# Kernel optimization log

Hardware: AMD Instinct MI355X
Metric: run time of the kernel (lower is better)

## Reference

```python
import jax, jax.numpy as jnp
import numpy as np

NUM_HEADS = 16
WINDOW = 256  # window_size: each query i attends to keys [max(0, i-W+1), i]


def setup_inputs() -> dict:
    key = jax.random.key(0)
    k1, k2, k3, k4, k5 = jax.random.split(key, 5)
    B, S, D = 2, 4096, 1024
    scale = 0.02
    return {
        "x": jax.random.normal(k1, (B, S, D), dtype=jnp.float32),
        "wq": jax.random.normal(k2, (D, D), dtype=jnp.float32) * scale,
        "wk": jax.random.normal(k3, (D, D), dtype=jnp.float32) * scale,
        "wv": jax.random.normal(k4, (D, D), dtype=jnp.float32) * scale,
        "wo": jax.random.normal(k5, (D, D), dtype=jnp.float32) * scale,
    }


def _sliding_window_attn(x, wq, wk, wv, wo):
    B, S, D = x.shape
    H, W = NUM_HEADS, WINDOW
    Dh = D // H
    nb = S // W  # number of query blocks (S assumed divisible by W)

    def proj(w):
        # nn.Linear: y = x @ w.T ; -> [B, H, nb, W, Dh]
        y = (x @ w.T).reshape(B, nb, W, H, Dh)
        return y.transpose(0, 3, 1, 2, 4)

    q = proj(wq)
    k = proj(wk)
    v = proj(wv)

    # Each query block j attends to key blocks j-1 and j (banded causal window).
    zpad = jnp.zeros((B, H, 1, W, Dh), dtype=x.dtype)
    kpad = jnp.concatenate([zpad, k], axis=2)  # [B,H,nb+1,W,Dh]
    vpad = jnp.concatenate([zpad, v], axis=2)
    k2 = jnp.concatenate([kpad[:, :, :-1], kpad[:, :, 1:]], axis=3)  # [B,H,nb,2W,Dh]
    v2 = jnp.concatenate([vpad[:, :, :-1], vpad[:, :, 1:]], axis=3)

    scores = jnp.einsum("bhjqd,bhjkd->bhjqk", q, k2) / jnp.sqrt(
        jnp.asarray(Dh, dtype=x.dtype)
    )  # [B,H,nb,W,2W]

    # Mask: query global pos i = j*W + qi; key global pos kp = (j-1)*W + ki.
    # Valid iff i-W+1 <= kp <= i  <=>  qi+1 <= ki <= qi+W ; and kp >= 0.
    qi = jnp.arange(W)[:, None]          # [W,1]
    ki = jnp.arange(2 * W)[None, :]      # [1,2W]
    band = (ki >= qi + 1) & (ki <= qi + W)                      # [W,2W]
    kpos_ok = (jnp.arange(nb)[:, None, None] - 1) * W + ki[None] >= 0  # [nb,1,2W]
    mask = band[None] & kpos_ok          # [nb,W,2W]

    neg = jnp.finfo(scores.dtype).min
    scores = jnp.where(mask[None, None], scores, neg)
    attn = jax.nn.softmax(scores, axis=-1)

    out = jnp.einsum("bhjqk,bhjkd->bhjqd", attn, v2)  # [B,H,nb,W,Dh]
    out = out.transpose(0, 2, 3, 1, 4).reshape(B, S, D)
    return out @ wo.T


def reference(x, wq, wk, wv, wo):
    return _sliding_window_attn(x, wq, wk, wv, wo)
```

## Files before the change

kernel.cpp:

```cpp
#include <hip/hip_runtime.h>

#define S_LEN 4096
#define DMODEL 1024
#define NH 16
#define DH 64
#define WIN 256
#define NQKV 3072

typedef __attribute__((ext_vector_type(8))) short short8;
typedef __attribute__((ext_vector_type(4))) short sh4;
typedef __attribute__((ext_vector_type(4))) float floatx4;

__device__ __forceinline__ ushort f2bf(float f) {
    union { float f; unsigned int i; } x;
    x.f = f;
    unsigned int r = x.i + 0x7FFFu + ((x.i >> 16) & 1u);
    return (ushort)(r >> 16);
}

__global__ __launch_bounds__(256) void cvt_bf16(const float* __restrict__ src,
                                                ushort* __restrict__ dst, int n8) {
    int i = blockIdx.x * 256 + threadIdx.x;
    if (i >= n8) return;
    const float* s = src + (size_t)i * 8;
    floatx4 f0 = *(const floatx4*)s;
    floatx4 f1 = *(const floatx4*)(s + 4);
    short8 v;
#pragma unroll
    for (int e = 0; e < 4; ++e) v[e] = (short)f2bf(f0[e]);
#pragma unroll
    for (int e = 0; e < 4; ++e) v[4 + e] = (short)f2bf(f1[e]);
    *(short8*)(dst + (size_t)i * 8) = v;
}

template <bool OUTF32>
__global__ __launch_bounds__(256) void gemm_bf16(const ushort* __restrict__ A,
                                                 const ushort* __restrict__ W,
                                                 void* __restrict__ Cout,
                                                 int M, int N, int K) {
    __shared__ __align__(16) ushort As[128 * 32];
    __shared__ __align__(16) ushort Ws[128 * 32];

    const int tid = threadIdx.x;
    const int w = tid >> 6, l = tid & 63;
    const int bm0 = blockIdx.y * 128, bn0 = blockIdx.x * 128;
    const int wm = (w >> 1) * 64, wn = (w & 1) * 64;
    const int lm = l & 15, lq = (l >> 4) * 8;

    floatx4 acc[4][4] = {};

    const int boff0 = w * 1024 + l * 16;
    const int boff1 = boff0 + 4096;
    const int r0 = boff0 >> 6, c0 = (boff0 & 63) >> 1;
    const int r1 = boff1 >> 6, c1 = (boff1 & 63) >> 1;

    const ushort* a0 = A + (size_t)(bm0 + r0) * K + c0;
    const ushort* a1 = A + (size_t)(bm0 + r1) * K + c1;
    const ushort* w0 = W + (size_t)(bn0 + r0) * K + c0;
    const ushort* w1 = W + (size_t)(bn0 + r1) * K + c1;

    for (int k0 = 0; k0 < K; k0 += 32) {
        __builtin_amdgcn_global_load_lds(
            (const __attribute__((address_space(1))) void*)(a0 + k0),
            (__attribute__((address_space(3))) void*)(As + (boff0 >> 1)), 16, 0, 0);
        __builtin_amdgcn_global_load_lds(
            (const __attribute__((address_space(1))) void*)(a1 + k0),
            (__attribute__((address_space(3))) void*)(As + (boff1 >> 1)), 16, 0, 0);
        __builtin_amdgcn_global_load_lds(
            (const __attribute__((address_space(1))) void*)(w0 + k0),
            (__attribute__((address_space(3))) void*)(Ws + (boff0 >> 1)), 16, 0, 0);
        __builtin_amdgcn_global_load_lds(
            (const __attribute__((address_space(1))) void*)(w1 + k0),
            (__attribute__((address_space(3))) void*)(Ws + (boff1 >> 1)), 16, 0, 0);
        __syncthreads();

        short8 af[4], wf[4];
#pragma unroll
        for (int mi = 0; mi < 4; ++mi)
            af[mi] = *(const short8*)&As[(wm + mi * 16 + lm) * 32 + lq];
#pragma unroll
        for (int ni = 0; ni < 4; ++ni)
            wf[ni] = *(const short8*)&Ws[(wn + ni * 16 + lm) * 32 + lq];
#pragma unroll
        for (int mi = 0; mi < 4; ++mi)
#pragma unroll
            for (int ni = 0; ni < 4; ++ni)
                acc[mi][ni] = __builtin_amdgcn_mfma_f32_16x16x32_bf16(
                    af[mi], wf[ni], acc[mi][ni], 0, 0, 0);
        __syncthreads();
    }

#pragma unroll
    for (int mi = 0; mi < 4; ++mi) {
#pragma unroll
        for (int ni = 0; ni < 4; ++ni) {
#pragma unroll
            for (int r = 0; r < 4; ++r) {
                int row = bm0 + wm + mi * 16 + (l >> 4) * 4 + r;
                int col = bn0 + wn + ni * 16 + lm;
                if (OUTF32)
                    ((float*)Cout)[(size_t)row * N + col] = acc[mi][ni][r];
                else
                    ((ushort*)Cout)[(size_t)row * N + col] = f2bf(acc[mi][ni][r]);
            }
        }
    }
}

#define KSP 72
#define VTP 136
#define PSP 40

__global__ __launch_bounds__(256) void swattn_mfma(const ushort* __restrict__ QKV,
                                                   ushort* __restrict__ O) {
    __shared__ __align__(16) ushort Ks[128 * KSP];
    __shared__ __align__(16) ushort Vt[64 * VTP];
    __shared__ __align__(16) ushort Ps[4 * 64 * PSP];
    __shared__ __align__(16) float lW[256];

    const int j = blockIdx.x, h = blockIdx.y, b = blockIdx.z;
    const int tid = threadIdx.x;
    const int w = tid >> 6, l = tid & 63;
    const int quad = l >> 4, lc = l & 15;

    const size_t base = (size_t)b * S_LEN * NQKV + (size_t)h * DH;
    const ushort* Qp = QKV + base;
    const ushort* Kp = QKV + base + DMODEL;
    const ushort* Vp = QKV + base + 2 * DMODEL;

    short8 qf[4][2];
#pragma unroll
    for (int nq = 0; nq < 4; ++nq)
#pragma unroll
        for (int kk = 0; kk < 2; ++kk)
            qf[nq][kk] = *(const short8*)(Qp +
                (size_t)(j * 256 + w * 64 + nq * 16 + lc) * NQKV + kk * 32 + quad * 8);

    floatx4 o[4][4] = {};
    float lsum[4] = {0.f, 0.f, 0.f, 0.f};

    const float sscale = 0.18033688011112042f;
    const float M0 = 2.0f;
    const int qlo = w * 64, qhi = w * 64 + 63;

    for (int c = 0; c < 4; ++c) {
        const int kg0 = (j - 1) * 256 + c * 128;
        if (kg0 < 0) continue;
        __syncthreads();
#pragma unroll
        for (int i = 0; i < 4; ++i) {
            int cc = i * 256 + tid, key = cc >> 3, seg = cc & 7;
            *(short8*)&Ks[key * KSP + seg * 8] =
                *(const short8*)(Kp + (size_t)(kg0 + key) * NQKV + seg * 8);
            short8 vv = *(const short8*)(Vp + (size_t)(kg0 + key) * NQKV + seg * 8);
#pragma unroll
            for (int e = 0; e < 8; ++e)
                Vt[(seg * 8 + e) * VTP + key] = (ushort)vv[e];
        }
        __syncthreads();

        const int krel0 = c * 128 - 256;
#pragma unroll
        for (int g = 0; g < 4; ++g) {
            const int k0 = krel0 + g * 32;
            if (k0 > qhi || k0 + 31 < qlo - 255) continue;

            floatx4 st[2][4];
            const floatx4 zero = {};
#pragma unroll
            for (int kt = 0; kt < 2; ++kt) {
                short8 kf0 = *(const short8*)&Ks[(g * 32 + kt * 16 + lc) * KSP + quad * 8];
                short8 kf1 = *(const short8*)&Ks[(g * 32 + kt * 16 + lc) * KSP + 32 + quad * 8];
#pragma unroll
                for (int nq = 0; nq < 4; ++nq) {
                    st[kt][nq] = __builtin_amdgcn_mfma_f32_16x16x32_bf16(kf0, qf[nq][0], zero, 0, 0, 0);
                    st[kt][nq] = __builtin_amdgcn_mfma_f32_16x16x32_bf16(kf1, qf[nq][1], st[kt][nq], 0, 0, 0);
                }
            }
#pragma unroll
            for (int kt = 0; kt < 2; ++kt)
#pragma unroll
                for (int nq = 0; nq < 4; ++nq) {
                    sh4 pv;
#pragma unroll
                    for (int r = 0; r < 4; ++r) {
                        int krel = k0 + kt * 16 + quad * 4 + r;
                        int qrel = qlo + nq * 16 + lc;
                        bool valid = (krel <= qrel) && (krel + 255 >= qrel);
                        float p = valid ? exp2f(st[kt][nq][r] * sscale - M0) : 0.f;
                        lsum[nq] += p;
                        pv[r] = (short)f2bf(p);
                    }
                    *(sh4*)&Ps[w * 64 * PSP + (nq * 16 + lc) * PSP + kt * 16 + quad * 4] = pv;
                }
            __threadfence_block();

            short8 vf[4];
#pragma unroll
            for (int nd = 0; nd < 4; ++nd)
                vf[nd] = *(const short8*)&Vt[(nd * 16 + lc) * VTP + g * 32 + quad * 8];
#pragma unroll
            for (int mq = 0; mq < 4; ++mq) {
                short8 pf = *(const short8*)&Ps[w * 64 * PSP + (mq * 16 + lc) * PSP + quad * 8];
#pragma unroll
                for (int nd = 0; nd < 4; ++nd)
                    o[mq][nd] = __builtin_amdgcn_mfma_f32_16x16x32_bf16(pf, vf[nd], o[mq][nd], 0, 0, 0);
            }
            __threadfence_block();
        }
    }

#pragma unroll
    for (int nq = 0; nq < 4; ++nq) {
        lsum[nq] += __shfl_xor(lsum[nq], 16);
        lsum[nq] += __shfl_xor(lsum[nq], 32);
    }
    if (l < 16) {
#pragma unroll
        for (int nq = 0; nq < 4; ++nq) lW[w * 64 + nq * 16 + l] = lsum[nq];
    }
    __threadfence_block();
#pragma unroll
    for (int mq = 0; mq < 4; ++mq) {
        floatx4 lv = *(const floatx4*)&lW[w * 64 + mq * 16 + quad * 4];
#pragma unroll
        for (int r = 0; r < 4; ++r) {
            float inv = 1.f / lv[r];
            int token = j * 256 + w * 64 + mq * 16 + quad * 4 + r;
#pragma unroll
            for (int nd = 0; nd < 4; ++nd)
                O[(size_t)b * S_LEN * DMODEL + (size_t)token * DMODEL + h * DH + nd * 16 + lc] =
                    f2bf(o[mq][nd][r] * inv);
        }
    }
}

extern "C" void kernel_launch(void* const* d_in, const int* in_sizes, int n_in,
                              void* d_out, int out_size, void* d_ws, size_t ws_size,
                              hipStream_t stream) {
    const float* x  = (const float*)d_in[0];
    const float* wq = (const float*)d_in[1];
    const float* wk = (const float*)d_in[2];
    const float* wv = (const float*)d_in[3];
    const float* wo = (const float*)d_in[4];
    float* out = (float*)d_out;

    const int D = DMODEL;
    const int M = in_sizes[0] / D;
    const int Bb = M / S_LEN;

    ushort* xb   = (ushort*)d_ws;
    ushort* W3b  = xb + (size_t)M * D;
    ushort* wob  = W3b + (size_t)NQKV * D;
    ushort* QKVb = wob + (size_t)D * D;
    ushort* Ob   = xb;

    const int nW = D * D;
    cvt_bf16<<<dim3((M * D / 8 + 255) / 256), dim3(256), 0, stream>>>(x, xb, M * D / 8);
    cvt_bf16<<<dim3((nW / 8 + 255) / 256), dim3(256), 0, stream>>>(wq, W3b, nW / 8);
    cvt_bf16<<<dim3((nW / 8 + 255) / 256), dim3(256), 0, stream>>>(wk, W3b + nW, nW / 8);
    cvt_bf16<<<dim3((nW / 8 + 255) / 256), dim3(256), 0, stream>>>(wv, W3b + 2 * nW, nW / 8);
    cvt_bf16<<<dim3((nW / 8 + 255) / 256), dim3(256), 0, stream>>>(wo, wob, nW / 8);

    gemm_bf16<false><<<dim3(NQKV / 128, M / 128), dim3(256), 0, stream>>>(
        xb, W3b, QKVb, M, NQKV, D);

    swattn_mfma<<<dim3(S_LEN / WIN, NH, Bb), dim3(256), 0, stream>>>(QKVb, Ob);

    gemm_bf16<true><<<dim3(D / 128, M / 128), dim3(256), 0, stream>>>(
        Ob, wob, out, M, D, D);
}
```

Measured before the change: 246.6 us.

## Fuse bf16 conversions into one launch and XOR-swizzle GEMM LDS tiles

```diff
diff --git a/kernel.cpp b/kernel.cpp
--- a/kernel.cpp
+++ b/kernel.cpp
@@ -18,19 +18,36 @@
     return (ushort)(r >> 16);
 }
 
-__global__ __launch_bounds__(256) void cvt_bf16(const float* __restrict__ src,
-                                                ushort* __restrict__ dst, int n8) {
+__global__ __launch_bounds__(256) void cvt_all(const float* __restrict__ x,
+                                               const float* __restrict__ wq,
+                                               const float* __restrict__ wk,
+                                               const float* __restrict__ wv,
+                                               const float* __restrict__ wo,
+                                               ushort* __restrict__ xb,
+                                               ushort* __restrict__ W3b,
+                                               ushort* __restrict__ wob,
+                                               int nx8, int nw8) {
     int i = blockIdx.x * 256 + threadIdx.x;
-    if (i >= n8) return;
-    const float* s = src + (size_t)i * 8;
-    floatx4 f0 = *(const floatx4*)s;
-    floatx4 f1 = *(const floatx4*)(s + 4);
+    const float* src;
+    ushort* dst;
+    if (i < nx8) {
+        src = x + (size_t)i * 8;            dst = xb + (size_t)i * 8;
+    } else {
+        int j = i - nx8;
+        int which = j / nw8, r = j - which * nw8;
+        if (which >= 4) return;
+        const float* w4[4] = {wq, wk, wv, wo};
+        src = w4[which] + (size_t)r * 8;
+        dst = (which == 3 ? wob : W3b + (size_t)which * nw8 * 8) + (size_t)r * 8;
+    }
+    floatx4 f0 = *(const floatx4*)src;
+    floatx4 f1 = *(const floatx4*)(src + 4);
     short8 v;
 #pragma unroll
     for (int e = 0; e < 4; ++e) v[e] = (short)f2bf(f0[e]);
 #pragma unroll
     for (int e = 0; e < 4; ++e) v[4 + e] = (short)f2bf(f1[e]);
-    *(short8*)(dst + (size_t)i * 8) = v;
+    *(short8*)dst = v;
 }
 
 template <bool OUTF32>
@@ -45,42 +62,43 @@
     const int w = tid >> 6, l = tid & 63;
     const int bm0 = blockIdx.y * 128, bn0 = blockIdx.x * 128;
     const int wm = (w >> 1) * 64, wn = (w & 1) * 64;
-    const int lm = l & 15, lq = (l >> 4) * 8;
+    const int lm = l & 15, quad = l >> 4;
 
     floatx4 acc[4][4] = {};
 
-    const int boff0 = w * 1024 + l * 16;
-    const int boff1 = boff0 + 4096;
-    const int r0 = boff0 >> 6, c0 = (boff0 & 63) >> 1;
-    const int r1 = boff1 >> 6, c1 = (boff1 & 63) >> 1;
-
-    const ushort* a0 = A + (size_t)(bm0 + r0) * K + c0;
-    const ushort* a1 = A + (size_t)(bm0 + r1) * K + c1;
-    const ushort* w0 = W + (size_t)(bn0 + r0) * K + c0;
-    const ushort* w1 = W + (size_t)(bn0 + r1) * K + c1;
+    const int row0 = tid >> 2;
+    const int gseg = (tid & 3) ^ (row0 & 3) ^ ((row0 >> 2) & 3);
+
+    const ushort* a0 = A + (size_t)(bm0 + row0) * K + gseg * 8;
+    const ushort* a1 = A + (size_t)(bm0 + row0 + 64) * K + gseg * 8;
+    const ushort* w0 = W + (size_t)(bn0 + row0) * K + gseg * 8;
+    const ushort* w1 = W + (size_t)(bn0 + row0 + 64) * K + gseg * 8;
+
+    const int swzl = (lm & 3) ^ ((lm >> 2) & 3);
 
     for (int k0 = 0; k0 < K; k0 += 32) {
         __builtin_amdgcn_global_load_lds(
             (const __attribute__((address_space(1))) void*)(a0 + k0),
-            (__attribute__((address_space(3))) void*)(As + (boff0 >> 1)), 16, 0, 0);
+            (__attribute__((address_space(3))) void*)(As + tid * 8), 16, 0, 0);
         __builtin_amdgcn_global_load_lds(
             (const __attribute__((address_space(1))) void*)(a1 + k0),
-            (__attribute__((address_space(3))) void*)(As + (boff1 >> 1)), 16, 0, 0);
+            (__attribute__((address_space(3))) void*)(As + 2048 + tid * 8), 16, 0, 0);
         __builtin_amdgcn_global_load_lds(
             (const __attribute__((address_space(1))) void*)(w0 + k0),
-            (__attribute__((address_space(3))) void*)(Ws + (boff0 >> 1)), 16, 0, 0);
+            (__attribute__((address_space(3))) void*)(Ws + tid * 8), 16, 0, 0);
         __builtin_amdgcn_global_load_lds(
             (const __attribute__((address_space(1))) void*)(w1 + k0),
-            (__attribute__((address_space(3))) void*)(Ws + (boff1 >> 1)), 16, 0, 0);
+            (__attribute__((address_space(3))) void*)(Ws + 2048 + tid * 8), 16, 0, 0);
         __syncthreads();
 
         short8 af[4], wf[4];
+        const int sseg = (quad ^ swzl) * 8;
 #pragma unroll
         for (int mi = 0; mi < 4; ++mi)
-            af[mi] = *(const short8*)&As[(wm + mi * 16 + lm) * 32 + lq];
+            af[mi] = *(const short8*)&As[(wm + mi * 16 + lm) * 32 + sseg];
 #pragma unroll
         for (int ni = 0; ni < 4; ++ni)
-            wf[ni] = *(const short8*)&Ws[(wn + ni * 16 + lm) * 32 + lq];
+            wf[ni] = *(const short8*)&Ws[(wn + ni * 16 + lm) * 32 + sseg];
 #pragma unroll
         for (int mi = 0; mi < 4; ++mi)
 #pragma unroll
@@ -96,7 +114,7 @@
         for (int ni = 0; ni < 4; ++ni) {
 #pragma unroll
             for (int r = 0; r < 4; ++r) {
-                int row = bm0 + wm + mi * 16 + (l >> 4) * 4 + r;
+                int row = bm0 + wm + mi * 16 + quad * 4 + r;
                 int col = bn0 + wn + ni * 16 + lm;
                 if (OUTF32)
                     ((float*)Cout)[(size_t)row * N + col] = acc[mi][ni][r];
@@ -255,12 +273,10 @@
     ushort* QKVb = wob + (size_t)D * D;
     ushort* Ob   = xb;
 
-    const int nW = D * D;
-    cvt_bf16<<<dim3((M * D / 8 + 255) / 256), dim3(256), 0, stream>>>(x, xb, M * D / 8);
-    cvt_bf16<<<dim3((nW / 8 + 255) / 256), dim3(256), 0, stream>>>(wq, W3b, nW / 8);
-    cvt_bf16<<<dim3((nW / 8 + 255) / 256), dim3(256), 0, stream>>>(wk, W3b + nW, nW / 8);
-    cvt_bf16<<<dim3((nW / 8 + 255) / 256), dim3(256), 0, stream>>>(wv, W3b + 2 * nW, nW / 8);
-    cvt_bf16<<<dim3((nW / 8 + 255) / 256), dim3(256), 0, stream>>>(wo, wob, nW / 8);
+    const int nx8 = M * D / 8, nw8 = D * D / 8;
+    const int ntot = nx8 + 4 * nw8;
+    cvt_all<<<dim3((ntot + 255) / 256), dim3(256), 0, stream>>>(
+        x, wq, wk, wv, wo, xb, W3b, wob, nx8, nw8);
 
     gemm_bf16<false><<<dim3(NQKV / 128, M / 128), dim3(256), 0, stream>>>(
         xb, W3b, QKVb, M, NQKV, D);
```

Result: no change. 246.0 us (-0.2%).
